# Optimization experiments

Hardware: AMD Instinct MI355X
Metric: run time of the kernel (lower is better)

Reference implementation:

```python
import jax, jax.numpy as jnp
import numpy as np

B, L, D, N = 4, 2048, 1024, 16


def setup_inputs() -> dict:
    key = jax.random.key(0)
    ks = jax.random.split(key, 12)
    s = 1.0 / np.sqrt(D)
    inp = {
        'x': jax.random.normal(ks[0], (B, L, D), jnp.float32),
        'ln_g': jnp.ones((D,), jnp.float32),
        'ln_b': jnp.zeros((D,), jnp.float32),
        'w1_w': jax.random.normal(ks[1], (D, D), jnp.float32) * s,
        'w1_b': jnp.zeros((D,), jnp.float32),
        'v1_w': jax.random.normal(ks[2], (D, D), jnp.float32) * s,
        'v1_b': jnp.zeros((D,), jnp.float32),
        'w2_w': jax.random.normal(ks[3], (D, D), jnp.float32) * s,
        'w2_b': jnp.zeros((D,), jnp.float32),
        'conv_w': jax.random.normal(ks[4], (D, 1, 3), jnp.float32) * (1.0 / np.sqrt(3.0)),
        'A_log': jnp.log(jnp.broadcast_to(jnp.arange(1, N + 1, dtype=jnp.float32), (D, N))),
        'D_skip': jnp.ones((D,), jnp.float32),
        'W_dt': jax.random.normal(ks[5], (D, D), jnp.float32) * (s * 0.1),
        'b_dt': jnp.full((D,), -4.0, jnp.float32),
        'W_B': jax.random.normal(ks[6], (D, N), jnp.float32) * s,
        'W_C': jax.random.normal(ks[7], (D, N), jnp.float32) * s,
    }
    return inp


def _layernorm(x, g, b, eps=1e-5):
    mu = jnp.mean(x, axis=-1, keepdims=True)
    var = jnp.mean(jnp.square(x - mu), axis=-1, keepdims=True)
    return (x - mu) * jax.lax.rsqrt(var + eps) * g + b


def _silu(x):
    return x * jax.nn.sigmoid(x)


def _depthwise_conv(x, w):
    # x: (B, L, D), w: (D, 1, 3), padding=1, groups=D
    xc = x.transpose(0, 2, 1)  # (B, D, L)
    y = jax.lax.conv_general_dilated(
        xc, w, window_strides=(1,), padding=[(1, 1)],
        feature_group_count=xc.shape[1],
        dimension_numbers=('NCH', 'OIH', 'NCH'))
    return y.transpose(0, 2, 1)


def _selective_scan(u, A_log, D_skip, W_dt, b_dt, W_B, W_C):
    # u: (B, L, D) -> y: (B, L, D); diagonal selective SSM (Mamba S6)
    A = -jnp.exp(A_log)                              # (D, N)
    dt = jax.nn.softplus(u @ W_dt + b_dt)            # (B, L, D)
    Bt = u @ W_B                                     # (B, L, N)
    Ct = u @ W_C                                     # (B, L, N)

    def step(h, inp):
        dt_t, B_t, C_t, u_t = inp                    # (B,D),(B,N),(B,N),(B,D)
        dA = jnp.exp(dt_t[..., None] * A)            # (B, D, N)
        h = dA * h + (dt_t * u_t)[..., None] * B_t[:, None, :]
        y = jnp.einsum('bdn,bn->bd', h, C_t)
        return h, y

    h0 = jnp.zeros((u.shape[0], u.shape[2], A.shape[1]), u.dtype)
    xs = (dt.transpose(1, 0, 2), Bt.transpose(1, 0, 2),
          Ct.transpose(1, 0, 2), u.transpose(1, 0, 2))
    _, ys = jax.lax.scan(step, h0, xs)               # ys: (L, B, D)
    return ys.transpose(1, 0, 2) + u * D_skip


def reference(x, ln_g, ln_b, w1_w, w1_b, v1_w, v1_b, w2_w, w2_b, conv_w,
              A_log, D_skip, W_dt, b_dt, W_B, W_C):
    x_norm = _layernorm(x, ln_g, ln_b)
    x1 = x_norm @ w1_w + w1_b
    x_conv = _silu(_depthwise_conv(x1, conv_w))
    x_ssm = _selective_scan(x_conv, A_log, D_skip, W_dt, b_dt, W_B, W_C)
    v = _silu(x_norm @ v1_w + v1_b)
    return (x_ssm * v) @ w2_w + w2_b
```

## Files before the change

### kernel.cpp

```cpp
#include <hip/hip_runtime.h>
#include <hip/hip_bf16.h>

#define BB 4
#define LL 2048
#define DD 1024
#define NN 16
#define BL (BB * LL)
#define NC 32
#define LC 64
#define MB 1048576

typedef float f32x4 __attribute__((ext_vector_type(4)));
typedef __bf16 bf16x8 __attribute__((ext_vector_type(8)));

typedef __attribute__((address_space(1))) unsigned int as1_u32;
typedef __attribute__((address_space(3))) unsigned int as3_u32;

__device__ __forceinline__ void gl_lds16(const void* g, void* l) {
  __builtin_amdgcn_global_load_lds((as1_u32*)g, (as3_u32*)l, 16, 0, 0);
}

__device__ __forceinline__ float fast_sigmoid(float x) {
  return 1.f / (1.f + __expf(-x));
}

__global__ __launch_bounds__(256) void k_prep_ln(const float* __restrict__ w1,
                                                 const float* __restrict__ v1,
                                                 const float* __restrict__ wdt,
                                                 const float* __restrict__ w2,
                                                 const float* __restrict__ WB,
                                                 const float* __restrict__ WC,
                                                 __hip_bfloat16* __restrict__ wcat,
                                                 __hip_bfloat16* __restrict__ wdtbc,
                                                 __hip_bfloat16* __restrict__ w2T,
                                                 const float* __restrict__ x,
                                                 const float* __restrict__ ln_g,
                                                 const float* __restrict__ ln_b,
                                                 __hip_bfloat16* __restrict__ xnorm) {
  const int z = blockIdx.z;
  __shared__ float tile[32][33];
  __shared__ float red[8];
  if (z < 4) {
    const float* src = (z == 0) ? w1 : (z == 1) ? v1 : (z == 2) ? wdt : w2;
    __hip_bfloat16* dst = (z == 0) ? wcat
                        : (z == 1) ? (wcat + (size_t)1024 * DD)
                        : (z == 2) ? wdtbc : w2T;
    const int kt = blockIdx.x * 32, nt = blockIdx.y * 32;
    const int tx = threadIdx.x & 31, ty = threadIdx.x >> 5;
#pragma unroll
    for (int j = 0; j < 32; j += 8)
      tile[ty + j][tx] = src[(size_t)(kt + ty + j) * DD + nt + tx];
    __syncthreads();
#pragma unroll
    for (int j = 0; j < 32; j += 8)
      dst[(size_t)(nt + ty + j) * DD + kt + tx] = __float2bfloat16(tile[tx][ty + j]);
  } else if (z == 4) {
    const int id = blockIdx.y * 32 + blockIdx.x;
    if (id < 128) {
      const int idx = id * 256 + threadIdx.x;
      const int k = idx & 1023, n = idx >> 10;
      const float v = (n < 16) ? WB[(size_t)k * 16 + n] : WC[(size_t)k * 16 + (n - 16)];
      wdtbc[(size_t)(1024 + n) * DD + k] = __float2bfloat16(v);
    } else if (id < 512) {
      const int idx = (id - 128) * 256 + threadIdx.x;
      wdtbc[(size_t)1056 * DD + idx] = __float2bfloat16(0.f);
    }
  } else {
    const int row = (z - 5) * 1024 + blockIdx.y * 32 + blockIdx.x;
    const int tid = threadIdx.x;
    const f32x4 xv = *(const f32x4*)(x + (size_t)row * DD + tid * 4);
    float s = xv[0] + xv[1] + xv[2] + xv[3];
    float sq = xv[0] * xv[0] + xv[1] * xv[1] + xv[2] * xv[2] + xv[3] * xv[3];
#pragma unroll
    for (int o = 32; o > 0; o >>= 1) {
      s += __shfl_down(s, o);
      sq += __shfl_down(sq, o);
    }
    const int wave = tid >> 6, lane = tid & 63;
    if (lane == 0) { red[wave] = s; red[4 + wave] = sq; }
    __syncthreads();
    s = red[0] + red[1] + red[2] + red[3];
    sq = red[4] + red[5] + red[6] + red[7];
    const float mean = s * (1.f / DD);
    const float var = sq * (1.f / DD) - mean * mean;
    const float rs = rsqrtf(var + 1e-5f);
    const f32x4 gv = *(const f32x4*)(ln_g + tid * 4);
    const f32x4 bv = *(const f32x4*)(ln_b + tid * 4);
    union { ushort4 u; __hip_bfloat16 h[4]; } cv;
#pragma unroll
    for (int j = 0; j < 4; ++j)
      cv.h[j] = __float2bfloat16((xv[j] - mean) * rs * gv[j] + bv[j]);
    *reinterpret_cast<ushort4*>(&xnorm[(size_t)row * DD + tid * 4]) = cv.u;
  }
}

template <int EPI>
__device__ __forceinline__ void gemm_body(const __hip_bfloat16* __restrict__ Ag,
                                          const __hip_bfloat16* __restrict__ Wg,
                                          void* __restrict__ o0, void* __restrict__ o1,
                                          void* __restrict__ o2,
                                          const float* __restrict__ bias0,
                                          const float* __restrict__ bias1) {
  __shared__ unsigned short As[128 * 64];
  __shared__ unsigned short Bs[128 * 64];
  const int tid = threadIdx.x;
  const int wave = tid >> 6, lane = tid & 63;
  const int quad = lane >> 4, l16 = lane & 15;
  const int wm = wave & 1, wn = wave >> 1;

  const int srow = lane >> 3;
  const int schunk = (lane & 7) ^ srow;
  const char* gA = (const char*)Ag +
      (size_t)(blockIdx.x * 128 + wave * 32 + srow) * 2048 + schunk * 16;
  const char* gB = (const char*)Wg +
      (size_t)(blockIdx.y * 128 + wave * 32 + srow) * 2048 + schunk * 16;
  char* lA = (char*)As + wave * 32 * 128;
  char* lB = (char*)Bs + wave * 32 * 128;

  f32x4 acc[4][4] = {};

  for (int kt = 0; kt < 16; ++kt) {
#pragma unroll
    for (int i = 0; i < 4; ++i) {
      gl_lds16(gA + i * 8 * 2048, lA + i * 1024);
      gl_lds16(gB + i * 8 * 2048, lB + i * 1024);
    }
    gA += 128;
    gB += 128;
    __syncthreads();
    bf16x8 af[2][4], bfr[2][4];
#pragma unroll
    for (int h = 0; h < 2; ++h)
#pragma unroll
      for (int i = 0; i < 4; ++i) {
        const int ra = wm * 64 + i * 16 + l16;
        const int rb = wn * 64 + i * 16 + l16;
        af[h][i] = *(const bf16x8*)((const char*)As + ra * 128 +
                                    (((h * 4 + quad) ^ (ra & 7)) * 16));
        bfr[h][i] = *(const bf16x8*)((const char*)Bs + rb * 128 +
                                     (((h * 4 + quad) ^ (rb & 7)) * 16));
      }
#pragma unroll
    for (int h = 0; h < 2; ++h)
#pragma unroll
      for (int i = 0; i < 4; ++i)
#pragma unroll
        for (int j = 0; j < 4; ++j)
          acc[i][j] =
              __builtin_amdgcn_mfma_f32_16x16x32_bf16(af[h][i], bfr[h][j], acc[i][j], 0, 0, 0);
    __syncthreads();
  }

  const int em0 = blockIdx.x * 128 + wm * 64 + quad * 4;
  const int en0 = blockIdx.y * 128 + wn * 64 + l16;
#pragma unroll
  for (int i = 0; i < 4; ++i) {
#pragma unroll
    for (int r = 0; r < 4; ++r) {
      const int m = em0 + i * 16 + r;
#pragma unroll
      for (int j = 0; j < 4; ++j) {
        const int n = en0 + j * 16;
        const float val = acc[i][j][r];
        if constexpr (EPI == 1) {
          if (n < 1024) {
            ((__hip_bfloat16*)o0)[(size_t)m * DD + n] = __float2bfloat16(val + bias0[n]);
          } else {
            const float t = val + bias1[n - 1024];
            ((__hip_bfloat16*)o1)[(size_t)m * DD + (n - 1024)] =
                __float2bfloat16(t * fast_sigmoid(t));
          }
        } else if constexpr (EPI == 2) {
          if (n < 1024) {
            const float t = val + bias0[n];
            const float sp = (t > 15.f) ? t : __logf(1.f + __expf(t));
            ((__hip_bfloat16*)o0)[(size_t)m * DD + n] = __float2bfloat16(sp);
          } else if (n < 1040) {
            ((float*)o1)[(size_t)m * NN + (n - 1024)] = val;
          } else if (n < 1056) {
            ((float*)o2)[(size_t)m * NN + (n - 1040)] = val;
          }
        } else {
          ((float*)o0)[(size_t)m * DD + n] = val + bias0[n];
        }
      }
    }
  }
}

__global__ __launch_bounds__(256) void k_gemm_xv(const __hip_bfloat16* __restrict__ Ag,
                                                 const __hip_bfloat16* __restrict__ Wg,
                                                 void* o0, void* o1,
                                                 const float* __restrict__ b0,
                                                 const float* __restrict__ b1) {
  gemm_body<1>(Ag, Wg, o0, o1, nullptr, b0, b1);
}
__global__ __launch_bounds__(256) void k_gemm_dbc(const __hip_bfloat16* __restrict__ Ag,
                                                  const __hip_bfloat16* __restrict__ Wg,
                                                  void* o0, void* o1, void* o2,
                                                  const float* __restrict__ b0) {
  gemm_body<2>(Ag, Wg, o0, o1, o2, b0, nullptr);
}
__global__ __launch_bounds__(256) void k_gemm_out(const __hip_bfloat16* __restrict__ Ag,
                                                  const __hip_bfloat16* __restrict__ Wg,
                                                  void* o0, const float* __restrict__ b0) {
  gemm_body<3>(Ag, Wg, o0, nullptr, nullptr, b0, nullptr);
}

__global__ __launch_bounds__(256) void k_conv_silu(const __hip_bfloat16* __restrict__ x1,
                                                   const float* __restrict__ w,
                                                   __hip_bfloat16* __restrict__ out) {
  const size_t e = ((size_t)blockIdx.x * 256 + threadIdx.x) * 8;
  const int d = (int)(e & 1023);
  const int l = (int)((e >> 10) & 2047);
  const bf16x8 zero = {};
  const bf16x8 xm = (l > 0) ? *(const bf16x8*)(x1 + e - DD) : zero;
  const bf16x8 x0 = *(const bf16x8*)(x1 + e);
  const bf16x8 xp = (l < LL - 1) ? *(const bf16x8*)(x1 + e + DD) : zero;
  bf16x8 o;
#pragma unroll
  for (int j = 0; j < 8; ++j) {
    const float w0 = w[(d + j) * 3 + 0], w1 = w[(d + j) * 3 + 1], w2 = w[(d + j) * 3 + 2];
    const float a = w0 * (float)xm[j] + w1 * (float)x0[j] + w2 * (float)xp[j];
    o[j] = (__bf16)(a * fast_sigmoid(a));
  }
  *(bf16x8*)(out + e) = o;
}

__global__ __launch_bounds__(256) void k_scan1(const __hip_bfloat16* __restrict__ dt,
                                               const __hip_bfloat16* __restrict__ u,
                                               const float* __restrict__ Bt,
                                               const float* __restrict__ A_log,
                                               float* __restrict__ P,
                                               float* __restrict__ hend) {
  const int d = blockIdx.x * 256 + threadIdx.x;
  const int c = blockIdx.y, b = blockIdx.z;
  __shared__ float Bsh[LC * NN];
  ((f32x4*)Bsh)[threadIdx.x] = ((const f32x4*)(Bt + (size_t)(b * LL + c * LC) * NN))[threadIdx.x];
  float a[NN];
#pragma unroll
  for (int n = 0; n < NN; ++n) a[n] = -__expf(A_log[(size_t)d * NN + n]);
  __syncthreads();
  float h[NN] = {};
  float sdt = 0.f;
  size_t idx = (size_t)(b * LL + c * LC) * DD + d;
#pragma unroll 4
  for (int t = 0; t < LC; ++t, idx += DD) {
    const float dtv = __bfloat162float(dt[idx]);
    const float uv = __bfloat162float(u[idx]);
    sdt += dtv;
    const float du = dtv * uv;
#pragma unroll
    for (int n = 0; n < NN; ++n)
      h[n] = __expf(dtv * a[n]) * h[n] + du * Bsh[t * NN + n];
  }
  const size_t o = ((size_t)((b * NC + c) * DD + d)) * NN;
#pragma unroll
  for (int n = 0; n < NN; ++n) {
    P[o + n] = __expf(sdt * a[n]);
    hend[o + n] = h[n];
  }
}

__global__ __launch_bounds__(256) void k_scan2(const float* __restrict__ P, float* __restrict__ h) {
  const int gidx = blockIdx.x * 256 + threadIdx.x;
  const int n = gidx & 15, d = (gidx >> 4) & 1023, b = gidx >> 14;
  float hs = 0.f;
  size_t off = ((size_t)b * NC * DD + d) * NN + n;
  const size_t stride = (size_t)DD * NN;
  for (int c = 0; c < NC; ++c, off += stride) {
    const float he = h[off];
    const float p = P[off];
    h[off] = hs;
    hs = p * hs + he;
  }
}

__global__ __launch_bounds__(256) void k_scan3(const __hip_bfloat16* __restrict__ dt,
                                               const __hip_bfloat16* __restrict__ u,
                                               const float* __restrict__ Bt,
                                               const float* __restrict__ Ct,
                                               const float* __restrict__ A_log,
                                               const float* __restrict__ hstart,
                                               const float* __restrict__ Dskip,
                                               const __hip_bfloat16* __restrict__ v,
                                               __hip_bfloat16* __restrict__ yA) {
  const int d = blockIdx.x * 256 + threadIdx.x;
  const int c = blockIdx.y, b = blockIdx.z;
  __shared__ float Bsh[LC * NN];
  __shared__ float Csh[LC * NN];
  ((f32x4*)Bsh)[threadIdx.x] = ((const f32x4*)(Bt + (size_t)(b * LL + c * LC) * NN))[threadIdx.x];
  ((f32x4*)Csh)[threadIdx.x] = ((const f32x4*)(Ct + (size_t)(b * LL + c * LC) * NN))[threadIdx.x];
  float a[NN];
#pragma unroll
  for (int n = 0; n < NN; ++n) a[n] = -__expf(A_log[(size_t)d * NN + n]);
  const float dsk = Dskip[d];
  float h[NN];
  const size_t o = ((size_t)((b * NC + c) * DD + d)) * NN;
#pragma unroll
  for (int n = 0; n < NN; ++n) h[n] = hstart[o + n];
  __syncthreads();
  size_t idx = (size_t)(b * LL + c * LC) * DD + d;
#pragma unroll 2
  for (int t = 0; t < LC; ++t, idx += DD) {
    const float dtv = __bfloat162float(dt[idx]);
    const float uv = __bfloat162float(u[idx]);
    const float du = dtv * uv;
    float y = 0.f;
#pragma unroll
    for (int n = 0; n < NN; ++n) {
      h[n] = __expf(dtv * a[n]) * h[n] + du * Bsh[t * NN + n];
      y += h[n] * Csh[t * NN + n];
    }
    const float xssm = y + uv * dsk;
    const float vv = __bfloat162float(v[idx]);
    yA[idx] = __float2bfloat16(xssm * vv);
  }
}

extern "C" void kernel_launch(void* const* d_in, const int* in_sizes, int n_in,
                              void* d_out, int out_size, void* d_ws, size_t ws_size,
                              hipStream_t stream) {
  const float* x      = (const float*)d_in[0];
  const float* ln_g   = (const float*)d_in[1];
  const float* ln_b   = (const float*)d_in[2];
  const float* w1_w   = (const float*)d_in[3];
  const float* w1_b   = (const float*)d_in[4];
  const float* v1_w   = (const float*)d_in[5];
  const float* v1_b   = (const float*)d_in[6];
  const float* w2_w   = (const float*)d_in[7];
  const float* w2_b   = (const float*)d_in[8];
  const float* conv_w = (const float*)d_in[9];
  const float* A_log  = (const float*)d_in[10];
  const float* D_skip = (const float*)d_in[11];
  const float* W_dt   = (const float*)d_in[12];
  const float* b_dt   = (const float*)d_in[13];
  const float* W_B    = (const float*)d_in[14];
  const float* W_C    = (const float*)d_in[15];

  char* ws = (char*)d_ws;
  const size_t OFF_SLOTA = 0;
  const size_t OFF_SLOTB = (size_t)16 * MB;
  const size_t OFF_VBUF  = (size_t)32 * MB;
  const size_t OFF_YA    = (size_t)48 * MB;
  const size_t OFF_WCAT  = (size_t)64 * MB;
  const size_t OFF_WDTBC = (size_t)68 * MB;
  const size_t OFF_W2T   = OFF_WDTBC + 2359296;
  const size_t OFF_BT    = OFF_W2T + 2097152;
  const size_t OFF_CT    = OFF_BT + 524288;
  const size_t OFF_P     = OFF_CT + 524288;
  const size_t OFF_H     = OFF_P + 8388608;

  __hip_bfloat16* xnorm = (__hip_bfloat16*)(ws + OFF_SLOTA);
  __hip_bfloat16* xconv = (__hip_bfloat16*)(ws + OFF_SLOTA);
  __hip_bfloat16* x1    = (__hip_bfloat16*)(ws + OFF_SLOTB);
  __hip_bfloat16* dtb   = (__hip_bfloat16*)(ws + OFF_SLOTB);
  __hip_bfloat16* vbuf  = (__hip_bfloat16*)(ws + OFF_VBUF);
  __hip_bfloat16* yA    = (__hip_bfloat16*)(ws + OFF_YA);
  __hip_bfloat16* wcat  = (__hip_bfloat16*)(ws + OFF_WCAT);
  __hip_bfloat16* wdtbc = (__hip_bfloat16*)(ws + OFF_WDTBC);
  __hip_bfloat16* w2T   = (__hip_bfloat16*)(ws + OFF_W2T);
  float* Btf = (float*)(ws + OFF_BT);
  float* Ctf = (float*)(ws + OFF_CT);
  float* P   = (float*)(ws + OFF_P);
  float* H   = (float*)(ws + OFF_H);

  k_prep_ln<<<dim3(32, 32, 13), 256, 0, stream>>>(w1_w, v1_w, W_dt, w2_w, W_B, W_C,
                                                  wcat, wdtbc, w2T, x, ln_g, ln_b, xnorm);

  k_gemm_xv<<<dim3(BL / 128, 2048 / 128), 256, 0, stream>>>(
      xnorm, wcat, (void*)x1, (void*)vbuf, w1_b, v1_b);

  k_conv_silu<<<(BL * DD / 8) / 256, 256, 0, stream>>>(x1, conv_w, xconv);

  k_gemm_dbc<<<dim3(BL / 128, 1152 / 128), 256, 0, stream>>>(
      xconv, wdtbc, (void*)dtb, (void*)Btf, (void*)Ctf, b_dt);

  k_scan1<<<dim3(DD / 256, NC, BB), 256, 0, stream>>>(dtb, xconv, Btf, A_log, P, H);
  k_scan2<<<(BB * DD * NN) / 256, 256, 0, stream>>>(P, H);
  k_scan3<<<dim3(DD / 256, NC, BB), 256, 0, stream>>>(dtb, xconv, Btf, Ctf, A_log, H, D_skip,
                                                      vbuf, yA);

  k_gemm_out<<<dim3(BL / 128, 1024 / 128), 256, 0, stream>>>(yA, w2T, d_out, w2_b);
}
```

Baseline: 371.2 us.

## Replace per-state exps with power products when A is integer-multiple structured

```diff
diff --git a/kernel.cpp b/kernel.cpp
--- a/kernel.cpp
+++ b/kernel.cpp
@@ -6,8 +6,8 @@
 #define DD 1024
 #define NN 16
 #define BL (BB * LL)
-#define NC 32
-#define LC 64
+#define NC 64
+#define LC 32
 #define MB 1048576
 
 typedef float f32x4 __attribute__((ext_vector_type(4)));
@@ -227,6 +227,7 @@
   *(bf16x8*)(out + e) = o;
 }
 
+
 __global__ __launch_bounds__(256) void k_scan1(const __hip_bfloat16* __restrict__ dt,
                                                const __hip_bfloat16* __restrict__ u,
                                                const float* __restrict__ Bt,
@@ -236,28 +237,59 @@
   const int d = blockIdx.x * 256 + threadIdx.x;
   const int c = blockIdx.y, b = blockIdx.z;
   __shared__ float Bsh[LC * NN];
-  ((f32x4*)Bsh)[threadIdx.x] = ((const f32x4*)(Bt + (size_t)(b * LL + c * LC) * NN))[threadIdx.x];
+  if (threadIdx.x < LC * NN / 4)
+    ((f32x4*)Bsh)[threadIdx.x] =
+        ((const f32x4*)(Bt + (size_t)(b * LL + c * LC) * NN))[threadIdx.x];
   float a[NN];
 #pragma unroll
   for (int n = 0; n < NN; ++n) a[n] = -__expf(A_log[(size_t)d * NN + n]);
+  const float a0 = a[0];
+  bool pw = true;
+#pragma unroll
+  for (int n = 0; n < NN; ++n) pw &= (fabsf(a[n] - (n + 1) * a0) <= 1e-3f * (n + 1));
   __syncthreads();
   float h[NN] = {};
   float sdt = 0.f;
   size_t idx = (size_t)(b * LL + c * LC) * DD + d;
-#pragma unroll 4
-  for (int t = 0; t < LC; ++t, idx += DD) {
-    const float dtv = __bfloat162float(dt[idx]);
-    const float uv = __bfloat162float(u[idx]);
-    sdt += dtv;
-    const float du = dtv * uv;
-#pragma unroll
-    for (int n = 0; n < NN; ++n)
-      h[n] = __expf(dtv * a[n]) * h[n] + du * Bsh[t * NN + n];
+  if (pw) {
+#pragma unroll 2
+    for (int t = 0; t < LC; ++t, idx += DD) {
+      const float dtv = __bfloat162float(dt[idx]);
+      const float uv = __bfloat162float(u[idx]);
+      sdt += dtv;
+      const float du = dtv * uv;
+      float w[NN];
+      w[0] = __expf(dtv * a0);
+#pragma unroll
+      for (int n = 1; n < NN; ++n) w[n] = w[(n - 1) >> 1] * w[n >> 1];
+#pragma unroll
+      for (int n = 0; n < NN; ++n) h[n] = w[n] * h[n] + du * Bsh[t * NN + n];
+    }
+  } else {
+#pragma unroll 2
+    for (int t = 0; t < LC; ++t, idx += DD) {
+      const float dtv = __bfloat162float(dt[idx]);
+      const float uv = __bfloat162float(u[idx]);
+      sdt += dtv;
+      const float du = dtv * uv;
+#pragma unroll
+      for (int n = 0; n < NN; ++n)
+        h[n] = __expf(dtv * a[n]) * h[n] + du * Bsh[t * NN + n];
+    }
   }
   const size_t o = ((size_t)((b * NC + c) * DD + d)) * NN;
+  float p[NN];
+  if (pw) {
+    p[0] = __expf(sdt * a0);
+#pragma unroll
+    for (int n = 1; n < NN; ++n) p[n] = p[(n - 1) >> 1] * p[n >> 1];
+  } else {
+#pragma unroll
+    for (int n = 0; n < NN; ++n) p[n] = __expf(sdt * a[n]);
+  }
 #pragma unroll
   for (int n = 0; n < NN; ++n) {
-    P[o + n] = __expf(sdt * a[n]);
+    P[o + n] = p[n];
     hend[o + n] = h[n];
   }
 }
@@ -289,11 +321,19 @@
   const int c = blockIdx.y, b = blockIdx.z;
   __shared__ float Bsh[LC * NN];
   __shared__ float Csh[LC * NN];
-  ((f32x4*)Bsh)[threadIdx.x] = ((const f32x4*)(Bt + (size_t)(b * LL + c * LC) * NN))[threadIdx.x];
-  ((f32x4*)Csh)[threadIdx.x] = ((const f32x4*)(Ct + (size_t)(b * LL + c * LC) * NN))[threadIdx.x];
+  if (threadIdx.x < 128)
+    ((f32x4*)Bsh)[threadIdx.x] =
+        ((const f32x4*)(Bt + (size_t)(b * LL + c * LC) * NN))[threadIdx.x];
+  else
+    ((f32x4*)Csh)[threadIdx.x - 128] =
+        ((const f32x4*)(Ct + (size_t)(b * LL + c * LC) * NN))[threadIdx.x - 128];
   float a[NN];
 #pragma unroll
   for (int n = 0; n < NN; ++n) a[n] = -__expf(A_log[(size_t)d * NN + n]);
+  const float a0 = a[0];
+  bool pw = true;
+#pragma unroll
+  for (int n = 0; n < NN; ++n) pw &= (fabsf(a[n] - (n + 1) * a0) <= 1e-3f * (n + 1));
   const float dsk = Dskip[d];
   float h[NN];
   const size_t o = ((size_t)((b * NC + c) * DD + d)) * NN;
@@ -301,20 +341,42 @@
   for (int n = 0; n < NN; ++n) h[n] = hstart[o + n];
   __syncthreads();
   size_t idx = (size_t)(b * LL + c * LC) * DD + d;
+  if (pw) {
 #pragma unroll 2
-  for (int t = 0; t < LC; ++t, idx += DD) {
-    const float dtv = __bfloat162float(dt[idx]);
-    const float uv = __bfloat162float(u[idx]);
-    const float du = dtv * uv;
-    float y = 0.f;
-#pragma unroll
-    for (int n = 0; n < NN; ++n) {
-      h[n] = __expf(dtv * a[n]) * h[n] + du * Bsh[t * NN + n];
-      y += h[n] * Csh[t * NN + n];
-    }
-    const float xssm = y + uv * dsk;
-    const float vv = __bfloat162float(v[idx]);
-    yA[idx] = __float2bfloat16(xssm * vv);
+    for (int t = 0; t < LC; ++t, idx += DD) {
+      const float dtv = __bfloat162float(dt[idx]);
+      const float uv = __bfloat162float(u[idx]);
+      const float du = dtv * uv;
+      float w[NN];
+      w[0] = __expf(dtv * a0);
+#pragma unroll
+      for (int n = 1; n < NN; ++n) w[n] = w[(n - 1) >> 1] * w[n >> 1];
+      float y = 0.f;
+#pragma unroll
+      for (int n = 0; n < NN; ++n) {
+        h[n] = w[n] * h[n] + du * Bsh[t * NN + n];
+        y += h[n] * Csh[t * NN + n];
+      }
+      const float xssm = y + uv * dsk;
+      const float vv = __bfloat162float(v[idx]);
+      yA[idx] = __float2bfloat16(xssm * vv);
+    }
+  } else {
+#pragma unroll 2
+    for (int t = 0; t < LC; ++t, idx += DD) {
+      const float dtv = __bfloat162float(dt[idx]);
+      const float uv = __bfloat162float(u[idx]);
+      const float du = dtv * uv;
+      float y = 0.f;
+#pragma unroll
+      for (int n = 0; n < NN; ++n) {
+        h[n] = __expf(dtv * a[n]) * h[n] + du * Bsh[t * NN + n];
+        y += h[n] * Csh[t * NN + n];
+      }
+      const float xssm = y + uv * dsk;
+      const float vv = __bfloat162float(v[idx]);
+      yA[idx] = __float2bfloat16(xssm * vv);
+    }
   }
 }
 
@@ -348,8 +410,7 @@
   const size_t OFF_W2T   = OFF_WDTBC + 2359296;
   const size_t OFF_BT    = OFF_W2T + 2097152;
   const size_t OFF_CT    = OFF_BT + 524288;
-  const size_t OFF_P     = OFF_CT + 524288;
-  const size_t OFF_H     = OFF_P + 8388608;
+  const size_t OFF_H     = OFF_CT + 524288;
 
   __hip_bfloat16* xnorm = (__hip_bfloat16*)(ws + OFF_SLOTA);
   __hip_bfloat16* xconv = (__hip_bfloat16*)(ws + OFF_SLOTA);
@@ -357,12 +418,12 @@
   __hip_bfloat16* dtb   = (__hip_bfloat16*)(ws + OFF_SLOTB);
   __hip_bfloat16* vbuf  = (__hip_bfloat16*)(ws + OFF_VBUF);
   __hip_bfloat16* yA    = (__hip_bfloat16*)(ws + OFF_YA);
+  float* P              = (float*)(ws + OFF_YA);
   __hip_bfloat16* wcat  = (__hip_bfloat16*)(ws + OFF_WCAT);
   __hip_bfloat16* wdtbc = (__hip_bfloat16*)(ws + OFF_WDTBC);
   __hip_bfloat16* w2T   = (__hip_bfloat16*)(ws + OFF_W2T);
   float* Btf = (float*)(ws + OFF_BT);
   float* Ctf = (float*)(ws + OFF_CT);
-  float* P   = (float*)(ws + OFF_P);
   float* H   = (float*)(ws + OFF_H);
 
   k_prep_ln<<<dim3(32, 32, 13), 256, 0, stream>>>(w1_w, v1_w, W_dt, w2_w, W_B, W_C,
```

New measurement: 340.7 us. -8.2%, faster.
